# Performance work log

Hardware: AMD Instinct MI355X
Metric: run time of the kernel (lower is better)

Reference implementation:

```python
import jax, jax.numpy as jnp
import numpy as np

B, S, H, NH, HD = 4, 4096, 1024, 16, 64

def setup_inputs() -> dict:
    key = jax.random.key(0)
    ks = jax.random.split(key, 5)
    scale = 1.0 / np.sqrt(H)
    return {
        "hidden_states": jax.random.normal(ks[0], (B, S, H), dtype=jnp.float32),
        "Wq": jax.random.normal(ks[1], (H, H), dtype=jnp.float32) * scale,
        "Wk": jax.random.normal(ks[2], (H, H), dtype=jnp.float32) * scale,
        "Wv": jax.random.normal(ks[3], (H, H), dtype=jnp.float32) * scale,
        "Wo": jax.random.normal(ks[4], (H, H), dtype=jnp.float32) * scale,
    }

def reference(hidden_states, Wq, Wk, Wv, Wo):
    b, s, h = hidden_states.shape
    # torch nn.Linear: y = x @ W.T
    q = (hidden_states @ Wq.T).reshape(b, s, NH, HD)
    k = (hidden_states @ Wk.T).reshape(b, s, NH, HD)
    v = (hidden_states @ Wv.T).reshape(b, s, NH, HD)
    # feature map: ELU (as in source, no +1)
    q = jax.nn.elu(q)
    k = jax.nn.elu(k)
    # per-head kv state: sum over sequence of outer products k_s v_s^T -> [b,h,d,e]
    kv = jnp.einsum('bshd,bshe->bhde', k, v)
    out = jnp.einsum('bqhd,bhde->bqhe', q, kv)  # [b,s,h,e]
    out = out.reshape(b, s, h)
    return out @ Wo.T  # dropout p=0.0 is identity
```

## Files before the change

kernel.cpp:

```cpp
#include <hip/hip_runtime.h>
#include <cstdint>
#include <cstddef>

#define B_  4
#define S_  4096
#define H_  1024
#define NH_ 16
#define M_  (B_*S_)

typedef __bf16 bf16x8 __attribute__((ext_vector_type(8)));
typedef float  f32x4  __attribute__((ext_vector_type(4)));

__device__ __forceinline__ unsigned short f2b(float f) {
  union { float f; unsigned u; } v; v.f = f;
  unsigned r = v.u + 0x7FFFu + ((v.u >> 16) & 1u);
  return (unsigned short)(r >> 16);
}
__device__ __forceinline__ float b2f(unsigned short u) {
  union { unsigned u; float f; } v; v.u = ((unsigned)u) << 16;
  return v.f;
}

#define GLD16(g, l) __builtin_amdgcn_global_load_lds( \
    (const __attribute__((address_space(1))) void*)(g), \
    (__attribute__((address_space(3))) void*)(l), 16, 0, 0)

#define VM(n)  asm volatile("s_waitcnt vmcnt(" #n ")" ::: "memory")
#define BAR()  do { asm volatile("" ::: "memory"); __builtin_amdgcn_s_barrier(); \
                    asm volatile("" ::: "memory"); } while (0)

__global__ void cast_f32_bf16(const float* __restrict__ src,
                              unsigned short* __restrict__ dst, int n4) {
  int i = blockIdx.x * blockDim.x + threadIdx.x;
  if (i >= n4) return;
  float4 f = reinterpret_cast<const float4*>(src)[i];
  ushort4 o;
  o.x = f2b(f.x); o.y = f2b(f.y); o.z = f2b(f.z); o.w = f2b(f.w);
  reinterpret_cast<ushort4*>(dst)[i] = o;
}

__global__ void cast_w4(const float* __restrict__ w0, const float* __restrict__ w1,
                        const float* __restrict__ w2, const float* __restrict__ w3,
                        unsigned short* __restrict__ dst) {
  int i = blockIdx.x * blockDim.x + threadIdx.x;
  int w = i >> 18, j = i & 0x3FFFF;
  const float* src = (w == 0) ? w0 : (w == 1) ? w1 : (w == 2) ? w2 : w3;
  float4 f = reinterpret_cast<const float4*>(src)[j];
  ushort4 o;
  o.x = f2b(f.x); o.y = f2b(f.y); o.z = f2b(f.z); o.w = f2b(f.w);
  reinterpret_cast<ushort4*>(dst)[i] = o;
}

template<int MODE>
__global__ __launch_bounds__(512, 2) void gemm256(
    const unsigned short* __restrict__ A_,
    const unsigned short* __restrict__ Bt_,
    void* __restrict__ out) {
  __shared__ __align__(16) unsigned short LDS[2][2][16384];

  const int NTN = (MODE == 0) ? 12 : 4;
  const int nx  = gridDim.x >> 3;
  const int b2  = (blockIdx.x & 7) * nx + (blockIdx.x >> 3);
  const int tileM = (b2 / NTN) << 8;
  const int tileN = (b2 % NTN) << 8;

  const unsigned short* Bt_e =
      (MODE == 1) ? (Bt_ + ((size_t)(tileM >> 12) << 20)) : Bt_;

  const int tid  = threadIdx.x;
  const int lane = tid & 63, wv = tid >> 6;
  const int wmi  = wv >> 2;
  const int wni  = wv & 3;
  const int fr   = lane & 15, fq = lane >> 4;

  const int sr0 = tid >> 3,          sc0 = (tid & 7) ^ (sr0 & 7);
  const int sr1 = (tid + 512) >> 3,  sc1 = (tid & 7) ^ (sr1 & 7);

#define STG(NB, ARR, HM, SRC, RB, TT) do {                                      \
    GLD16((SRC) + (size_t)((RB) + (HM)*128 + sr0) * 1024 + (TT)*64 + sc0*8,     \
          &LDS[NB][ARR][(HM)*8192 + wv*512]);                                   \
    GLD16((SRC) + (size_t)((RB) + (HM)*128 + sr1) * 1024 + (TT)*64 + sc1*8,     \
          &LDS[NB][ARR][(HM)*8192 + 4096 + wv*512]);                            \
  } while (0)

  f32x4 zero = {0.f, 0.f, 0.f, 0.f};
  f32x4 acc[2][2][4][2];
#pragma unroll
  for (int a = 0; a < 2; a++)
#pragma unroll
    for (int b = 0; b < 2; b++)
#pragma unroll
      for (int m = 0; m < 4; m++)
#pragma unroll
        for (int n = 0; n < 2; n++) acc[a][b][m][n] = zero;

#define PHASE(CB, MQ, NQ, ...) do {                                             \
    bf16x8 af[4][2], bv[2][2];                                                  \
    _Pragma("unroll")                                                           \
    for (int m = 0; m < 4; m++) {                                               \
      int r = (MQ)*128 + wmi*64 + m*16 + fr;                                    \
      af[m][0] = *(const bf16x8*)&LDS[CB][0][r*64 + (( fq   ) ^ (r&7))*8];      \
      af[m][1] = *(const bf16x8*)&LDS[CB][0][r*64 + ((4+fq  ) ^ (r&7))*8];      \
    }                                                                           \
    _Pragma("unroll")                                                           \
    for (int n = 0; n < 2; n++) {                                               \
      int r = (NQ)*128 + wni*32 + n*16 + fr;                                    \
      bv[n][0] = *(const bf16x8*)&LDS[CB][1][r*64 + (( fq   ) ^ (r&7))*8];      \
      bv[n][1] = *(const bf16x8*)&LDS[CB][1][r*64 + ((4+fq  ) ^ (r&7))*8];      \
    }                                                                           \
    __VA_ARGS__;                                                                \
    __builtin_amdgcn_s_setprio(1);                                              \
    _Pragma("unroll")                                                           \
    for (int m = 0; m < 4; m++)                                                 \
      _Pragma("unroll")                                                         \
      for (int n = 0; n < 2; n++) {                                             \
        acc[MQ][NQ][m][n] = __builtin_amdgcn_mfma_f32_16x16x32_bf16(            \
            af[m][0], bv[n][0], acc[MQ][NQ][m][n], 0, 0, 0);                    \
        acc[MQ][NQ][m][n] = __builtin_amdgcn_mfma_f32_16x16x32_bf16(            \
            af[m][1], bv[n][1], acc[MQ][NQ][m][n], 0, 0, 0);                    \
      }                                                                         \
    __builtin_amdgcn_s_setprio(0);                                              \
  } while (0)

  STG(0, 0, 0, A_,   tileM, 0);
  STG(0, 0, 1, A_,   tileM, 0);
  STG(0, 1, 0, Bt_e, tileN, 0);
  STG(0, 1, 1, Bt_e, tileN, 0);
  VM(0);
  BAR();

  int cb = 0;
  for (int t = 0; t < 15; ++t) {
    const int nb = cb ^ 1;
    PHASE(cb, 0, 0, STG(nb, 0, 0, A_, tileM, t + 1);
                    STG(nb, 1, 0, Bt_e, tileN, t + 1));
    VM(6); BAR();
    PHASE(cb, 0, 1, STG(nb, 1, 1, Bt_e, tileN, t + 1));
    VM(6); BAR();
    PHASE(cb, 1, 0, STG(nb, 0, 1, A_, tileM, t + 1));
    BAR();
    PHASE(cb, 1, 1, );
    VM(4); BAR();
    cb = nb;
  }
  PHASE(cb, 0, 0, );
  VM(2); BAR();
  PHASE(cb, 0, 1, );
  VM(0); BAR();
  PHASE(cb, 1, 0, );
  PHASE(cb, 1, 1, );

#pragma unroll
  for (int mq = 0; mq < 2; mq++)
#pragma unroll
    for (int nq = 0; nq < 2; nq++)
#pragma unroll
      for (int m = 0; m < 4; m++)
#pragma unroll
        for (int n = 0; n < 2; n++)
#pragma unroll
          for (int r = 0; r < 4; r++) {
            int row = tileM + mq * 128 + wmi * 64 + m * 16 + fq * 4 + r;
            int col = tileN + nq * 128 + wni * 32 + n * 16 + fr;
            float v = acc[mq][nq][m][n][r];
            if (MODE == 0) {
              int reg = col >> 10, lc = col & 1023;
              if (reg < 2) v = v > 0.f ? v : (expf(v) - 1.f);
              ((unsigned short*)out)[(size_t)reg * ((size_t)M_ * H_) +
                                     (size_t)row * H_ + lc] = f2b(v);
            } else {
              ((float*)out)[(size_t)row * H_ + col] = v;
            }
          }
#undef PHASE
#undef STG
}

__global__ __launch_bounds__(256) void kv_partial(
    const unsigned short* __restrict__ Kb,
    const unsigned short* __restrict__ Vb,
    float* __restrict__ kvp) {
  __shared__ __align__(16) unsigned short kt[32 * 64];
  __shared__ __align__(16) unsigned short vt[32 * 64];
  const int bh = blockIdx.x >> 3;
  const int ch = blockIdx.x & 7;
  const int b  = bh >> 4, h = bh & 15;
  const int t  = threadIdx.x;
  const int rr = t >> 3;
  const int cc = (t & 7) * 8;
  const int d0 = (t >> 4) * 4;
  const int e0 = (t & 15) * 4;

  float acc[4][4] = {};
  for (int s0 = ch * 512; s0 < ch * 512 + 512; s0 += 32) {
    size_t g = (size_t)(b * S_ + s0 + rr) * H_ + h * 64 + cc;
    *reinterpret_cast<uint4*>(&kt[rr * 64 + cc]) = *reinterpret_cast<const uint4*>(Kb + g);
    *reinterpret_cast<uint4*>(&vt[rr * 64 + cc]) = *reinterpret_cast<const uint4*>(Vb + g);
    __syncthreads();
#pragma unroll 4
    for (int ss = 0; ss < 32; ss++) {
      ushort4 k4 = *reinterpret_cast<const ushort4*>(&kt[ss * 64 + d0]);
      ushort4 v4 = *reinterpret_cast<const ushort4*>(&vt[ss * 64 + e0]);
      float kf[4] = {b2f(k4.x), b2f(k4.y), b2f(k4.z), b2f(k4.w)};
      float vf[4] = {b2f(v4.x), b2f(v4.y), b2f(v4.z), b2f(v4.w)};
#pragma unroll
      for (int i = 0; i < 4; i++)
#pragma unroll
        for (int j = 0; j < 4; j++) acc[i][j] += kf[i] * vf[j];
    }
    __syncthreads();
  }
  float* outp = kvp + (size_t)blockIdx.x * 4096;
#pragma unroll
  for (int i = 0; i < 4; i++)
#pragma unroll
    for (int j = 0; j < 4; j++) outp[(d0 + i) * 64 + e0 + j] = acc[i][j];
}

__global__ __launch_bounds__(256) void kv_reduce(
    const float* __restrict__ kvp, unsigned short* __restrict__ KVb) {
  const int bh = blockIdx.x;
#pragma unroll
  for (int i = 0; i < 16; i++) {
    int idx = threadIdx.x + i * 256;
    float s = 0.f;
#pragma unroll
    for (int ch = 0; ch < 8; ch++) s += kvp[(size_t)(bh * 8 + ch) * 4096 + idx];
    KVb[(size_t)bh * 4096 + idx] = f2b(s);
  }
}

__global__ __launch_bounds__(256) void merge_m(
    const unsigned short* __restrict__ KVb,
    const unsigned short* __restrict__ Wob,
    unsigned short* __restrict__ MbT) {
  const int bh = blockIdx.x >> 2;
  const int nc = blockIdx.x & 3;
  const int b  = bh >> 4, h = bh & 15;
  const int lane = threadIdx.x & 63, wv = threadIdx.x >> 6;
  const int fr = lane & 15, fq = lane >> 4;
  const int ncb = nc * 256 + wv * 64;

  f32x4 zero = {0.f, 0.f, 0.f, 0.f};
  f32x4 acc[4][4];
#pragma unroll
  for (int i = 0; i < 4; i++)
#pragma unroll
    for (int j = 0; j < 4; j++) acc[i][j] = zero;

#pragma unroll
  for (int kk = 0; kk < 2; kk++) {
    bf16x8 af[4], bv[4];
#pragma unroll
    for (int i = 0; i < 4; i++)
      af[i] = *(const bf16x8*)&KVb[(size_t)bh * 4096 + (i * 16 + fr) * 64 + kk * 32 + fq * 8];
#pragma unroll
    for (int j = 0; j < 4; j++)
      bv[j] = *(const bf16x8*)&Wob[(size_t)(ncb + j * 16 + fr) * 1024 + h * 64 + kk * 32 + fq * 8];
#pragma unroll
    for (int i = 0; i < 4; i++)
#pragma unroll
      for (int j = 0; j < 4; j++)
        acc[i][j] = __builtin_amdgcn_mfma_f32_16x16x32_bf16(af[i], bv[j], acc[i][j], 0, 0, 0);
  }
#pragma unroll
  for (int i = 0; i < 4; i++)
#pragma unroll
    for (int j = 0; j < 4; j++)
#pragma unroll
      for (int r = 0; r < 4; r++) {
        int n = ncb + j * 16 + fr;
        int k = h * 64 + i * 16 + fq * 4 + r;
        MbT[((size_t)b << 20) + (size_t)n * 1024 + k] = f2b(acc[i][j][r]);
      }
}

extern "C" void kernel_launch(void* const* d_in, const int* in_sizes, int n_in,
                              void* d_out, int out_size, void* d_ws, size_t ws_size,
                              hipStream_t stream) {
  (void)in_sizes; (void)n_in; (void)out_size; (void)ws_size;
  const float* X  = (const float*)d_in[0];
  const float* Wq = (const float*)d_in[1];
  const float* Wk = (const float*)d_in[2];
  const float* Wv = (const float*)d_in[3];
  const float* Wo = (const float*)d_in[4];

  char*  ws  = (char*)d_ws;
  size_t off = 0;
  auto alloc = [&](size_t bytes) -> char* {
    char* p = ws + off;
    off += (bytes + 255) & ~(size_t)255;
    return p;
  };
  unsigned short* Xb   = (unsigned short*)alloc((size_t)M_ * H_ * 2);
  unsigned short* Wcat = (unsigned short*)alloc((size_t)4 * H_ * H_ * 2);
  unsigned short* QKVb = (unsigned short*)alloc((size_t)3 * M_ * H_ * 2);
  float*          kvp  = (float*)alloc((size_t)64 * 8 * 4096 * 4);
  unsigned short* KVb  = (unsigned short*)alloc((size_t)64 * 4096 * 2);
  unsigned short* MbT  = (unsigned short*)alloc((size_t)4 * H_ * H_ * 2);

  unsigned short* Qb = QKVb;
  unsigned short* Kb = QKVb + (size_t)M_ * H_;
  unsigned short* Vb = QKVb + (size_t)2 * M_ * H_;
  unsigned short* Wob = Wcat + (size_t)3 * H_ * H_;

  cast_f32_bf16<<<(M_ * H_) / 1024, 256, 0, stream>>>(X, Xb, (M_ * H_) / 4);
  cast_w4<<<(4 * H_ * H_) / 1024, 256, 0, stream>>>(Wq, Wk, Wv, Wo, Wcat);

  gemm256<0><<<768, 512, 0, stream>>>(Xb, Wcat, QKVb);

  kv_partial<<<512, 256, 0, stream>>>(Kb, Vb, kvp);
  kv_reduce<<<64, 256, 0, stream>>>(kvp, KVb);
  merge_m<<<256, 256, 0, stream>>>(KVb, Wob, MbT);

  gemm256<1><<<256, 512, 0, stream>>>(Qb, MbT, (float*)d_out);
}
```

Before: 258.1 us.

## Restructure GEMM main loop into split LDS-load/MFMA phases and double kv_partial chunks

```diff
diff --git a/kernel.cpp b/kernel.cpp
--- a/kernel.cpp
+++ b/kernel.cpp
@@ -25,7 +25,7 @@
     (const __attribute__((address_space(1))) void*)(g), \
     (__attribute__((address_space(3))) void*)(l), 16, 0, 0)
 
-#define VM(n)  asm volatile("s_waitcnt vmcnt(" #n ")" ::: "memory")
+#define VM0()  asm volatile("s_waitcnt vmcnt(0)" ::: "memory")
 #define BAR()  do { asm volatile("" ::: "memory"); __builtin_amdgcn_s_barrier(); \
                     asm volatile("" ::: "memory"); } while (0)
 
@@ -83,32 +83,25 @@
           &LDS[NB][ARR][(HM)*8192 + 4096 + wv*512]);                            \
   } while (0)
 
-  f32x4 zero = {0.f, 0.f, 0.f, 0.f};
-  f32x4 acc[2][2][4][2];
-#pragma unroll
-  for (int a = 0; a < 2; a++)
-#pragma unroll
-    for (int b = 0; b < 2; b++)
-#pragma unroll
-      for (int m = 0; m < 4; m++)
-#pragma unroll
-        for (int n = 0; n < 2; n++) acc[a][b][m][n] = zero;
-
-#define PHASE(CB, MQ, NQ, ...) do {                                             \
-    bf16x8 af[4][2], bv[2][2];                                                  \
+#define LOADA(CB, MQ) do {                                                      \
     _Pragma("unroll")                                                           \
     for (int m = 0; m < 4; m++) {                                               \
       int r = (MQ)*128 + wmi*64 + m*16 + fr;                                    \
-      af[m][0] = *(const bf16x8*)&LDS[CB][0][r*64 + (( fq   ) ^ (r&7))*8];      \
-      af[m][1] = *(const bf16x8*)&LDS[CB][0][r*64 + ((4+fq  ) ^ (r&7))*8];      \
+      af[m][0] = *(const bf16x8*)&LDS[CB][0][r*64 + ((fq    ) ^ (r&7))*8];      \
+      af[m][1] = *(const bf16x8*)&LDS[CB][0][r*64 + ((4 + fq) ^ (r&7))*8];      \
     }                                                                           \
+  } while (0)
+
+#define LOADB(CB, NQ) do {                                                      \
     _Pragma("unroll")                                                           \
     for (int n = 0; n < 2; n++) {                                               \
       int r = (NQ)*128 + wni*32 + n*16 + fr;                                    \
-      bv[n][0] = *(const bf16x8*)&LDS[CB][1][r*64 + (( fq   ) ^ (r&7))*8];      \
-      bv[n][1] = *(const bf16x8*)&LDS[CB][1][r*64 + ((4+fq  ) ^ (r&7))*8];      \
+      bv[n][0] = *(const bf16x8*)&LDS[CB][1][r*64 + ((fq    ) ^ (r&7))*8];      \
+      bv[n][1] = *(const bf16x8*)&LDS[CB][1][r*64 + ((4 + fq) ^ (r&7))*8];      \
     }                                                                           \
-    __VA_ARGS__;                                                                \
+  } while (0)
+
+#define MM(MQ, NQ) do {                                                         \
     __builtin_amdgcn_s_setprio(1);                                              \
     _Pragma("unroll")                                                           \
     for (int m = 0; m < 4; m++)                                                 \
@@ -122,33 +115,52 @@
     __builtin_amdgcn_s_setprio(0);                                              \
   } while (0)
 
+  f32x4 zero = {0.f, 0.f, 0.f, 0.f};
+  f32x4 acc[2][2][4][2];
+#pragma unroll
+  for (int a = 0; a < 2; a++)
+#pragma unroll
+    for (int b = 0; b < 2; b++)
+#pragma unroll
+      for (int m = 0; m < 4; m++)
+#pragma unroll
+        for (int n = 0; n < 2; n++) acc[a][b][m][n] = zero;
+
+  bf16x8 af[4][2], bv[2][2];
+
   STG(0, 0, 0, A_,   tileM, 0);
   STG(0, 0, 1, A_,   tileM, 0);
   STG(0, 1, 0, Bt_e, tileN, 0);
   STG(0, 1, 1, Bt_e, tileN, 0);
-  VM(0);
+  VM0();
   BAR();
 
   int cb = 0;
   for (int t = 0; t < 15; ++t) {
     const int nb = cb ^ 1;
-    PHASE(cb, 0, 0, STG(nb, 0, 0, A_, tileM, t + 1);
-                    STG(nb, 1, 0, Bt_e, tileN, t + 1));
-    VM(6); BAR();
-    PHASE(cb, 0, 1, STG(nb, 1, 1, Bt_e, tileN, t + 1));
-    VM(6); BAR();
-    PHASE(cb, 1, 0, STG(nb, 0, 1, A_, tileM, t + 1));
-    BAR();
-    PHASE(cb, 1, 1, );
-    VM(4); BAR();
+    LOADA(cb, 0); LOADB(cb, 0);
+    STG(nb, 0, 0, A_,   tileM, t + 1);
+    STG(nb, 1, 0, Bt_e, tileN, t + 1);
+    BAR(); MM(0, 0); BAR();
+    LOADB(cb, 1);
+    STG(nb, 1, 1, Bt_e, tileN, t + 1);
+    BAR(); MM(0, 1); BAR();
+    LOADA(cb, 1);
+    STG(nb, 0, 1, A_,   tileM, t + 1);
+    BAR(); MM(1, 1); BAR();
+    LOADB(cb, 0);
+    VM0();
+    BAR(); MM(1, 0); BAR();
     cb = nb;
   }
-  PHASE(cb, 0, 0, );
-  VM(2); BAR();
-  PHASE(cb, 0, 1, );
-  VM(0); BAR();
-  PHASE(cb, 1, 0, );
-  PHASE(cb, 1, 1, );
+  LOADA(cb, 0); LOADB(cb, 0);
+  BAR(); MM(0, 0); BAR();
+  LOADB(cb, 1);
+  BAR(); MM(0, 1); BAR();
+  LOADA(cb, 1);
+  BAR(); MM(1, 1); BAR();
+  LOADB(cb, 0);
+  BAR(); MM(1, 0);
 
 #pragma unroll
   for (int mq = 0; mq < 2; mq++)
@@ -172,7 +184,9 @@
               ((float*)out)[(size_t)row * H_ + col] = v;
             }
           }
-#undef PHASE
+#undef MM
+#undef LOADB
+#undef LOADA
 #undef STG
 }
 
@@ -182,8 +196,8 @@
     float* __restrict__ kvp) {
   __shared__ __align__(16) unsigned short kt[32 * 64];
   __shared__ __align__(16) unsigned short vt[32 * 64];
-  const int bh = blockIdx.x >> 3;
-  const int ch = blockIdx.x & 7;
+  const int bh = blockIdx.x >> 4;
+  const int ch = blockIdx.x & 15;
   const int b  = bh >> 4, h = bh & 15;
   const int t  = threadIdx.x;
   const int rr = t >> 3;
@@ -192,7 +206,7 @@
   const int e0 = (t & 15) * 4;
 
   float acc[4][4] = {};
-  for (int s0 = ch * 512; s0 < ch * 512 + 512; s0 += 32) {
+  for (int s0 = ch * 256; s0 < ch * 256 + 256; s0 += 32) {
     size_t g = (size_t)(b * S_ + s0 + rr) * H_ + h * 64 + cc;
     *reinterpret_cast<uint4*>(&kt[rr * 64 + cc]) = *reinterpret_cast<const uint4*>(Kb + g);
     *reinterpret_cast<uint4*>(&vt[rr * 64 + cc]) = *reinterpret_cast<const uint4*>(Vb + g);
@@ -225,7 +239,7 @@
     int idx = threadIdx.x + i * 256;
     float s = 0.f;
 #pragma unroll
-    for (int ch = 0; ch < 8; ch++) s += kvp[(size_t)(bh * 8 + ch) * 4096 + idx];
+    for (int ch = 0; ch < 16; ch++) s += kvp[(size_t)(bh * 16 + ch) * 4096 + idx];
     KVb[(size_t)bh * 4096 + idx] = f2b(s);
   }
 }
@@ -250,18 +264,18 @@
 
 #pragma unroll
   for (int kk = 0; kk < 2; kk++) {
-    bf16x8 af[4], bv[4];
+    bf16x8 af[4], bvv[4];
 #pragma unroll
     for (int i = 0; i < 4; i++)
       af[i] = *(const bf16x8*)&KVb[(size_t)bh * 4096 + (i * 16 + fr) * 64 + kk * 32 + fq * 8];
 #pragma unroll
     for (int j = 0; j < 4; j++)
-      bv[j] = *(const bf16x8*)&Wob[(size_t)(ncb + j * 16 + fr) * 1024 + h * 64 + kk * 32 + fq * 8];
+      bvv[j] = *(const bf16x8*)&Wob[(size_t)(ncb + j * 16 + fr) * 1024 + h * 64 + kk * 32 + fq * 8];
 #pragma unroll
     for (int i = 0; i < 4; i++)
 #pragma unroll
       for (int j = 0; j < 4; j++)
-        acc[i][j] = __builtin_amdgcn_mfma_f32_16x16x32_bf16(af[i], bv[j], acc[i][j], 0, 0, 0);
+        acc[i][j] = __builtin_amdgcn_mfma_f32_16x16x32_bf16(af[i], bvv[j], acc[i][j], 0, 0, 0);
   }
 #pragma unroll
   for (int i = 0; i < 4; i++)
@@ -295,7 +309,7 @@
   unsigned short* Xb   = (unsigned short*)alloc((size_t)M_ * H_ * 2);
   unsigned short* Wcat = (unsigned short*)alloc((size_t)4 * H_ * H_ * 2);
   unsigned short* QKVb = (unsigned short*)alloc((size_t)3 * M_ * H_ * 2);
-  float*          kvp  = (float*)alloc((size_t)64 * 8 * 4096 * 4);
+  float*          kvp  = (float*)alloc((size_t)64 * 16 * 4096 * 4);
   unsigned short* KVb  = (unsigned short*)alloc((size_t)64 * 4096 * 2);
   unsigned short* MbT  = (unsigned short*)alloc((size_t)4 * H_ * H_ * 2);
 
@@ -309,7 +323,7 @@
 
   gemm256<0><<<768, 512, 0, stream>>>(Xb, Wcat, QKVb);
 
-  kv_partial<<<512, 256, 0, stream>>>(Kb, Vb, kvp);
+  kv_partial<<<1024, 256, 0, stream>>>(Kb, Vb, kvp);
   kv_reduce<<<64, 256, 0, stream>>>(kvp, KVb);
   merge_m<<<256, 256, 0, stream>>>(KVb, Wob, MbT);
 
```

Result: slower. 276.1 us (+7.0%).
